# Kernel optimization log

Measured on AMD Instinct MI355X. Metric: run time of the kernel, lower is better.

## Reference

```python
import jax, jax.numpy as jnp
import numpy as np
import math

B, S, D, H = 2, 2048, 768, 12
DK = D // H


def setup_inputs() -> dict:
    key = jax.random.key(0)
    ks = jax.random.split(key, 8)
    scale = 1.0 / math.sqrt(D)  # xavier-ish scale for weights
    inp = {
        "query": jax.random.normal(ks[0], (B, S, D), jnp.float32),
        "key": jax.random.normal(ks[1], (B, S, D), jnp.float32),
        "value": jax.random.normal(ks[2], (B, S, D), jnp.float32),
        # causal mask: True = masked (matches torch masked_fill_ semantics)
        "mask": jnp.broadcast_to(jnp.triu(jnp.ones((S, S), bool), k=1), (B, S, S)),
        "wq": jax.random.normal(ks[3], (D, D), jnp.float32) * scale,
        "wk": jax.random.normal(ks[4], (D, D), jnp.float32) * scale,
        "wv": jax.random.normal(ks[5], (D, D), jnp.float32) * scale,
        "wo": jax.random.normal(ks[6], (D, D), jnp.float32) * scale,
        "bo": jnp.zeros((D,), jnp.float32),
    }
    return inp


def reference(query, key, value, mask, wq, wk, wv, wo, bo):
    # nn.Linear stores weight [out, in]; y = x @ W^T
    def split_heads(x):  # [B,S,D] -> [B,H,S,DK]
        return x.reshape(B, S, H, DK).transpose(0, 2, 1, 3)

    q = split_heads(jnp.einsum('bsd,ed->bse', query, wq))
    k = split_heads(jnp.einsum('bsd,ed->bse', key, wk))
    v = split_heads(jnp.einsum('bsd,ed->bse', value, wv))

    scores = jnp.einsum('bhqd,bhkd->bhqk', q, k) / math.sqrt(DK)
    scores = jnp.where(mask[:, None, :, :], -jnp.inf, scores)
    attn = jax.nn.softmax(scores, axis=-1)  # dropout is identity in eval / p=0

    attended = jnp.einsum('bhqk,bhkd->bhqd', attn, v)
    attended = attended.transpose(0, 2, 1, 3).reshape(B, S, D)
    return jnp.einsum('bsd,ed->bse', attended, wo) + bo
```

## Files before the change

### kernel.cpp

```cpp
#include <hip/hip_runtime.h>

namespace {
constexpr int Sc = 2048, Dc = 768, Hc = 12, Mc = 4096;

using fragb = __attribute__((ext_vector_type(8))) short;
using f32x4 = __attribute__((ext_vector_type(4))) float;

#define MFMA16(A, B, C) __builtin_amdgcn_mfma_f32_16x16x32_bf16(A, B, C, 0, 0, 0)

__device__ __forceinline__ unsigned short bf16rne(float f) {
  unsigned int u = __float_as_uint(f);
  return (unsigned short)((u + 0x7fffu + ((u >> 16) & 1u)) >> 16);
}
__device__ __forceinline__ void splitt(float f, unsigned short& h, unsigned short& l) {
  const unsigned int u = __float_as_uint(f);
  h = (unsigned short)(u >> 16);
  const float r = f - __uint_as_float(u & 0xffff0000u);
  l = (unsigned short)(__float_as_uint(r) >> 16);
}
__device__ __forceinline__ void gload16(const unsigned short* g, unsigned short* l) {
  __builtin_amdgcn_global_load_lds(
      (const __attribute__((address_space(1))) void*)g,
      (__attribute__((address_space(3))) void*)l, 16, 0, 0);
}

__global__ __launch_bounds__(256) void split_kernel(
    const float* __restrict__ src, unsigned short* __restrict__ h,
    unsigned short* __restrict__ l, int n8)
{
  const int i = blockIdx.x * 256 + threadIdx.x;
  if (i >= n8) return;
  const float4 v0 = *(const float4*)(src + (size_t)i * 8);
  const float4 v1 = *(const float4*)(src + (size_t)i * 8 + 4);
  const float x[8] = {v0.x, v0.y, v0.z, v0.w, v1.x, v1.y, v1.z, v1.w};
  unsigned short hh[8], ll[8];
#pragma unroll
  for (int j = 0; j < 8; ++j) splitt(x[j], hh[j], ll[j]);
  *(uint4*)&h[(size_t)i * 8] = *(const uint4*)&hh[0];
  *(uint4*)&l[(size_t)i * 8] = *(const uint4*)&ll[0];
}

template <int OMODE>
__global__ __launch_bounds__(256, 4) void proj_kernel(
    const unsigned short* __restrict__ Xh, const unsigned short* __restrict__ Xl,
    const float* __restrict__ W, const float* __restrict__ bias,
    unsigned short* __restrict__ Oh, unsigned short* __restrict__ Ol,
    float* __restrict__ Ofp)
{
  const int tid = threadIdx.x;
  const int lane = tid & 63, w = tid >> 6;
  const int g = lane >> 4, l15 = lane & 15;
  const int lrow = lane >> 2, lslot = lane & 3;
  const int m0 = blockIdx.x * 128, n0 = blockIdx.y * 64;

  __shared__ __align__(16) unsigned short sb[12288];

  f32x4 acc[2][4] = {};

  const int brow = tid >> 2;
  const int bcol = (tid & 3) * 8;
  const float* wp0 = W + (size_t)(n0 + brow) * Dc + bcol;

  for (int k0 = 0; k0 < Dc; k0 += 32) {
    unsigned int bpk[4], lpk[4];
    {
      const float* wp = wp0 + k0;
      const float4 v0 = *(const float4*)wp;
      const float4 v1 = *(const float4*)(wp + 4);
      const float x[8] = {v0.x, v0.y, v0.z, v0.w, v1.x, v1.y, v1.z, v1.w};
#pragma unroll
      for (int j = 0; j < 4; ++j) {
        unsigned short h0, l0, h1, l1;
        splitt(x[2*j], h0, l0); splitt(x[2*j+1], h1, l1);
        bpk[j] = (unsigned int)h0 | ((unsigned int)h1 << 16);
        lpk[j] = (unsigned int)l0 | ((unsigned int)l1 << 16);
      }
    }
    __syncthreads();
#pragma unroll
    for (int i = 0; i < 2; ++i) {
      const int q = 2 * w + i;
      const size_t goff = (size_t)(m0 + q * 16 + lrow) * Dc + k0 + lslot * 8;
      gload16(Xh + goff, &sb[q * 512]);
      gload16(Xl + goff, &sb[4096 + q * 512]);
    }
    *(uint4*)&sb[8192  + brow * 32 + bcol] = *(const uint4*)&bpk[0];
    *(uint4*)&sb[10240 + brow * 32 + bcol] = *(const uint4*)&lpk[0];
    __syncthreads();

    fragb bHf[4], bLf[4];
#pragma unroll
    for (int nb = 0; nb < 4; ++nb) {
      bHf[nb] = *(const fragb*)&sb[8192  + (nb * 16 + l15) * 32 + 8 * g];
      bLf[nb] = *(const fragb*)&sb[10240 + (nb * 16 + l15) * 32 + 8 * g];
    }
#pragma unroll
    for (int s = 0; s < 2; ++s) {
      const fragb aH = *(const fragb*)&sb[(32 * w + 16 * s + l15) * 32 + 8 * g];
      const fragb aL = *(const fragb*)&sb[4096 + (32 * w + 16 * s + l15) * 32 + 8 * g];
#pragma unroll
      for (int nb = 0; nb < 4; ++nb) {
        acc[s][nb] = MFMA16(aH, bHf[nb], acc[s][nb]);
        acc[s][nb] = MFMA16(aH, bLf[nb], acc[s][nb]);
        acc[s][nb] = MFMA16(aL, bHf[nb], acc[s][nb]);
      }
    }
  }

  if constexpr (OMODE == 2) {
#pragma unroll
    for (int s = 0; s < 2; ++s) {
      const int mrow = m0 + 32 * w + 16 * s + 4 * g;
#pragma unroll
      for (int nb = 0; nb < 4; ++nb) {
        const int n = n0 + nb * 16 + l15;
        const float bv = bias[n];
#pragma unroll
        for (int r = 0; r < 4; ++r)
          Ofp[(size_t)(mrow + r) * Dc + n] = acc[s][nb][r] + bv;
      }
    }
  } else {
    const int hsel = n0 >> 6;
    const int bb = m0 >> 11;
    const int sl0 = m0 & (Sc - 1);
#pragma unroll
    for (int pass = 0; pass < 2; ++pass) {
      __syncthreads();
#pragma unroll
      for (int s = 0; s < 2; ++s)
#pragma unroll
        for (int nb = 0; nb < 4; ++nb)
#pragma unroll
          for (int r = 0; r < 4; ++r) {
            unsigned short hv, lv;
            splitt(acc[s][nb][r], hv, lv);
            const int srow = 32 * w + 16 * s + 4 * g + r;
            const int dk = nb * 16 + l15;
            if (OMODE == 0) sb[srow * 64 + dk] = pass ? lv : hv;
            else            sb[dk * 128 + srow] = pass ? lv : hv;
          }
      __syncthreads();
      unsigned short* dst = pass ? Ol : Oh;
#pragma unroll
      for (int c2 = tid; c2 < 1024; c2 += 256) {
        size_t gidx;
        if (OMODE == 0) {
          const int sl = c2 >> 3, off = (c2 & 7) * 8;
          gidx = (((size_t)bb * Hc + hsel) * Sc + sl0 + sl) * 64 + off;
        } else {
          const int dk = c2 >> 4, off = (c2 & 15) * 8;
          gidx = (((size_t)bb * Hc + hsel) * 64 + dk) * Sc + sl0 + off;
        }
        *(uint4*)&dst[gidx] = *(const uint4*)&sb[c2 * 8];
      }
    }
  }
}

__global__ __launch_bounds__(256, 3) void attn_kernel(
    const unsigned short* __restrict__ Qh, const unsigned short* __restrict__ Ql,
    const unsigned short* __restrict__ Kh, const unsigned short* __restrict__ Kl,
    const unsigned short* __restrict__ Vth, const unsigned short* __restrict__ Vtl,
    unsigned short* __restrict__ Aoh, unsigned short* __restrict__ Aol)
{
  const int tid = threadIdx.x;
  const int lane = tid & 63, w = tid >> 6;
  const int g = lane >> 4, l15 = lane & 15;
  const int lrow = lane >> 2, lslot = lane & 3;
  const int t = blockIdx.x;
  const int bh = blockIdx.y;
  const int b = bh / Hc, h = bh % Hc;

  const int qtile = (w < 2) ? t : (63 - t);
  const int qbase = qtile * 32 + (w & 1) * 16;
  const int ktmax = (qbase + 15) >> 6;
  const int NKT = ((Sc - 1 - 32 * t) >> 6) + 1;

  __shared__ __align__(16) unsigned short sbuf[20992];

  const unsigned short* gbase;
  if      (w == 0) gbase = Kh  + (size_t)bh * Sc * 64;
  else if (w == 1) gbase = Kl  + (size_t)bh * Sc * 64;
  else if (w == 2) gbase = Vth + (size_t)bh * 64 * Sc;
  else             gbase = Vtl + (size_t)bh * 64 * Sc;
  const bool isK = (w < 2);

  fragb qfh[2], qfl[2];
  {
    const unsigned short* qrh = Qh + ((size_t)bh * Sc + qbase + l15) * 64;
    const unsigned short* qrl = Ql + ((size_t)bh * Sc + qbase + l15) * 64;
#pragma unroll
    for (int c = 0; c < 2; ++c) {
      qfh[c] = *(const fragb*)(qrh + c * 32 + g * 8);
      qfl[c] = *(const fragb*)(qrl + c * 32 + g * 8);
    }
  }

  f32x4 oacc[4] = {};
  float m_run[4] = {-1e30f, -1e30f, -1e30f, -1e30f};
  float l_run[4] = {0.f, 0.f, 0.f, 0.f};

  for (int kt = 0; kt < NKT; ++kt) {
    const int k0 = kt * 64;
    __syncthreads();
#pragma unroll
    for (int q = 0; q < 8; ++q) {
      const int cc = q >> 2, rb = (q & 3) * 16;
      const size_t off = isK
          ? ((size_t)(k0 + rb + lrow) * 64 + cc * 32 + lslot * 8)
          : ((size_t)(rb + lrow) * Sc + k0 + cc * 32 + lslot * 8);
      gload16(gbase + off, &sbuf[w * 4096 + q * 512]);
    }
    __syncthreads();

    if (kt <= ktmax) {
      f32x4 sacc[4] = {};
#pragma unroll
      for (int c = 0; c < 2; ++c) {
#pragma unroll
        for (int kb = 0; kb < 4; ++kb) {
          const fragb kH = *(const fragb*)&sbuf[c * 2048 + (kb * 16 + l15) * 32 + g * 8];
          const fragb kL = *(const fragb*)&sbuf[4096 + c * 2048 + (kb * 16 + l15) * 32 + g * 8];
          sacc[kb] = MFMA16(qfh[c], kH, sacc[kb]);
          sacc[kb] = MFMA16(qfh[c], kL, sacc[kb]);
          sacc[kb] = MFMA16(qfl[c], kH, sacc[kb]);
        }
      }
      float p[4][4], mx[4];
#pragma unroll
      for (int r = 0; r < 4; ++r) {
        const int qrow = qbase + 4 * g + r;
#pragma unroll
        for (int kb = 0; kb < 4; ++kb) {
          const int kc = k0 + kb * 16 + l15;
          const float x = sacc[kb][r] * 0.125f;
          p[kb][r] = (kc > qrow) ? -1e30f : x;
        }
        mx[r] = fmaxf(fmaxf(p[0][r], p[1][r]), fmaxf(p[2][r], p[3][r]));
      }
#pragma unroll
      for (int off = 8; off > 0; off >>= 1)
#pragma unroll
        for (int r = 0; r < 4; ++r)
          mx[r] = fmaxf(mx[r], __shfl_xor(mx[r], off));
#pragma unroll
      for (int r = 0; r < 4; ++r) {
        const float mnew = fmaxf(m_run[r], mx[r]);
        const float alpha = __expf(m_run[r] - mnew);
        m_run[r] = mnew;
        float rs = 0.f;
#pragma unroll
        for (int kb = 0; kb < 4; ++kb) { p[kb][r] = __expf(p[kb][r] - mnew); rs += p[kb][r]; }
#pragma unroll
        for (int off = 8; off > 0; off >>= 1) rs += __shfl_xor(rs, off);
        l_run[r] = l_run[r] * alpha + rs;
#pragma unroll
        for (int db = 0; db < 4; ++db) oacc[db][r] *= alpha;
      }
      const int strip = 16 * w;
#pragma unroll
      for (int kb = 0; kb < 4; ++kb)
#pragma unroll
        for (int r = 0; r < 4; ++r)
          sbuf[16384 + (strip + 4 * g + r) * 72 + kb * 16 + l15] = bf16rne(p[kb][r]);
#pragma unroll
      for (int c = 0; c < 2; ++c) {
        const fragb pf = *(const fragb*)&sbuf[16384 + (strip + l15) * 72 + c * 32 + g * 8];
#pragma unroll
        for (int db = 0; db < 4; ++db) {
          const fragb vH = *(const fragb*)&sbuf[8192  + c * 2048 + (db * 16 + l15) * 32 + g * 8];
          const fragb vL = *(const fragb*)&sbuf[12288 + c * 2048 + (db * 16 + l15) * 32 + g * 8];
          oacc[db] = MFMA16(pf, vH, oacc[db]);
          oacc[db] = MFMA16(pf, vL, oacc[db]);
        }
      }
    }
  }

#pragma unroll
  for (int r = 0; r < 4; ++r) {
    const float rl = 1.0f / l_run[r];
    const int s = qbase + 4 * g + r;
    const size_t base = ((size_t)b * Sc + s) * Dc + h * 64 + l15;
#pragma unroll
    for (int db = 0; db < 4; ++db) {
      unsigned short hbits, lbits;
      splitt(oacc[db][r] * rl, hbits, lbits);
      Aoh[base + db * 16] = hbits;
      Aol[base + db * 16] = lbits;
    }
  }
}

}

extern "C" void kernel_launch(void* const* d_in, const int* in_sizes, int n_in,
                              void* d_out, int out_size, void* d_ws, size_t ws_size,
                              hipStream_t stream) {
  const float* q  = (const float*)d_in[0];
  const float* k  = (const float*)d_in[1];
  const float* v  = (const float*)d_in[2];
  const float* wq = (const float*)d_in[4];
  const float* wk = (const float*)d_in[5];
  const float* wv = (const float*)d_in[6];
  const float* wo = (const float*)d_in[7];
  const float* bo = (const float*)d_in[8];

  unsigned short* ws = (unsigned short*)d_ws;
  const size_t NQ = (size_t)Mc * Dc;
  unsigned short* Xh_  = ws + 0 * NQ;
  unsigned short* Xl_  = ws + 1 * NQ;
  unsigned short* Qh_  = ws + 2 * NQ;
  unsigned short* Ql_  = ws + 3 * NQ;
  unsigned short* Kh_  = ws + 4 * NQ;
  unsigned short* Kl_  = ws + 5 * NQ;
  unsigned short* Vth_ = ws + 6 * NQ;
  unsigned short* Vtl_ = ws + 7 * NQ;

  const dim3 blk(256);
  const dim3 gsplit((Mc * Dc / 8 + 255) / 256);
  const dim3 gproj(Mc / 128, Dc / 64);
  const dim3 gattn(32, 2 * Hc);

  split_kernel<<<gsplit, blk, 0, stream>>>(q, Xh_, Xl_, Mc * Dc / 8);
  proj_kernel<0><<<gproj, blk, 0, stream>>>(Xh_, Xl_, wq, nullptr, Qh_, Ql_, nullptr);
  split_kernel<<<gsplit, blk, 0, stream>>>(k, Xh_, Xl_, Mc * Dc / 8);
  proj_kernel<0><<<gproj, blk, 0, stream>>>(Xh_, Xl_, wk, nullptr, Kh_, Kl_, nullptr);
  split_kernel<<<gsplit, blk, 0, stream>>>(v, Xh_, Xl_, Mc * Dc / 8);
  proj_kernel<1><<<gproj, blk, 0, stream>>>(Xh_, Xl_, wv, nullptr, Vth_, Vtl_, nullptr);
  attn_kernel<<<gattn, blk, 0, stream>>>(Qh_, Ql_, Kh_, Kl_, Vth_, Vtl_, Xh_, Xl_);
  proj_kernel<2><<<gproj, blk, 0, stream>>>(Xh_, Xl_, wo, bo, nullptr, nullptr, (float*)d_out);
}
```

Before: 349.5 us.

## Double-buffer LDS staging, XOR-swizzle shared layouts, and remap blocks for cache locality

Both the projection and attention kernels now use two LDS buffers, so the next K-tile's global-to-LDS loads are issued before computing on the current tile, and each iteration needs one barrier instead of two. Shared-memory tiles and the output staging buffers use an XOR swizzle to cut bank conflicts, and the 1D grids are remapped so neighbouring blocks spread across the XCDs with better L2 reuse. This doubles LDS use and lowers the occupancy hints (proj 4 to 3, attn 3 to 2). The projection output mode becomes a runtime argument instead of a template parameter.

```diff
diff --git a/kernel.cpp b/kernel.cpp
--- a/kernel.cpp
+++ b/kernel.cpp
@@ -18,7 +18,7 @@
   const float r = f - __uint_as_float(u & 0xffff0000u);
   l = (unsigned short)(__float_as_uint(r) >> 16);
 }
-__device__ __forceinline__ void gload16(const unsigned short* g, unsigned short* l) {
+__device__ __forceinline__ void gload16(const void* g, unsigned short* l) {
   __builtin_amdgcn_global_load_lds(
       (const __attribute__((address_space(1))) void*)g,
       (__attribute__((address_space(3))) void*)l, 16, 0, 0);
@@ -40,64 +40,61 @@
   *(uint4*)&l[(size_t)i * 8] = *(const uint4*)&ll[0];
 }
 
-template <int OMODE>
-__global__ __launch_bounds__(256, 4) void proj_kernel(
+__global__ __launch_bounds__(256, 3) void proj_kernel(
     const unsigned short* __restrict__ Xh, const unsigned short* __restrict__ Xl,
     const float* __restrict__ W, const float* __restrict__ bias,
     unsigned short* __restrict__ Oh, unsigned short* __restrict__ Ol,
-    float* __restrict__ Ofp)
+    float* __restrict__ Ofp, int omode)
 {
   const int tid = threadIdx.x;
   const int lane = tid & 63, w = tid >> 6;
   const int g = lane >> 4, l15 = lane & 15;
-  const int lrow = lane >> 2, lslot = lane & 3;
-  const int m0 = blockIdx.x * 128, n0 = blockIdx.y * 64;
-
-  __shared__ __align__(16) unsigned short sb[12288];
+  const int ar4 = lane >> 2, as4 = lane & 3;
+  const int asw = as4 ^ ((ar4 >> 1) & 3);
+  const int selr = (l15 >> 1) & 3;
+
+  const int bid = blockIdx.x;
+  const int swz = (bid & 7) * 48 + (bid >> 3);
+  const int m0 = (swz / 12) * 128, n0 = (swz % 12) * 64;
+
+  __shared__ __align__(16) unsigned short sb[24576];
 
   f32x4 acc[2][4] = {};
 
   const int brow = tid >> 2;
-  const int bcol = (tid & 3) * 8;
-  const float* wp0 = W + (size_t)(n0 + brow) * Dc + bcol;
-
-  for (int k0 = 0; k0 < Dc; k0 += 32) {
-    unsigned int bpk[4], lpk[4];
-    {
-      const float* wp = wp0 + k0;
-      const float4 v0 = *(const float4*)wp;
-      const float4 v1 = *(const float4*)(wp + 4);
-      const float x[8] = {v0.x, v0.y, v0.z, v0.w, v1.x, v1.y, v1.z, v1.w};
-#pragma unroll
-      for (int j = 0; j < 4; ++j) {
-        unsigned short h0, l0, h1, l1;
-        splitt(x[2*j], h0, l0); splitt(x[2*j+1], h1, l1);
-        bpk[j] = (unsigned int)h0 | ((unsigned int)h1 << 16);
-        lpk[j] = (unsigned int)l0 | ((unsigned int)l1 << 16);
-      }
-    }
-    __syncthreads();
+  const int bslot = (tid & 3) ^ ((tid >> 3) & 3);
+  const float* wp0 = W + (size_t)(n0 + brow) * Dc + (tid & 3) * 8;
+
+  auto stageA = [&](int k0, int bufb) {
 #pragma unroll
     for (int i = 0; i < 2; ++i) {
       const int q = 2 * w + i;
-      const size_t goff = (size_t)(m0 + q * 16 + lrow) * Dc + k0 + lslot * 8;
-      gload16(Xh + goff, &sb[q * 512]);
-      gload16(Xl + goff, &sb[4096 + q * 512]);
-    }
-    *(uint4*)&sb[8192  + brow * 32 + bcol] = *(const uint4*)&bpk[0];
-    *(uint4*)&sb[10240 + brow * 32 + bcol] = *(const uint4*)&lpk[0];
-    __syncthreads();
-
+      const size_t goff = (size_t)(m0 + q * 16 + ar4) * Dc + k0 + asw * 8;
+      gload16(Xh + goff, &sb[bufb + q * 512]);
+      gload16(Xl + goff, &sb[bufb + 4096 + q * 512]);
+    }
+  };
+  auto writeB = [&](const float4& f0, const float4& f1, int bufb) {
+    const float x[8] = {f0.x, f0.y, f0.z, f0.w, f1.x, f1.y, f1.z, f1.w};
+    unsigned short hh[8], ll[8];
+#pragma unroll
+    for (int j = 0; j < 8; ++j) splitt(x[j], hh[j], ll[j]);
+    *(uint4*)&sb[bufb + 8192  + brow * 32 + bslot * 8] = *(const uint4*)&hh[0];
+    *(uint4*)&sb[bufb + 10240 + brow * 32 + bslot * 8] = *(const uint4*)&ll[0];
+  };
+  auto compute = [&](int bufb) {
     fragb bHf[4], bLf[4];
 #pragma unroll
     for (int nb = 0; nb < 4; ++nb) {
-      bHf[nb] = *(const fragb*)&sb[8192  + (nb * 16 + l15) * 32 + 8 * g];
-      bLf[nb] = *(const fragb*)&sb[10240 + (nb * 16 + l15) * 32 + 8 * g];
+      const int ro = (nb * 16 + l15) * 32 + ((g ^ selr) * 8);
+      bHf[nb] = *(const fragb*)&sb[bufb + 8192 + ro];
+      bLf[nb] = *(const fragb*)&sb[bufb + 10240 + ro];
     }
 #pragma unroll
     for (int s = 0; s < 2; ++s) {
-      const fragb aH = *(const fragb*)&sb[(32 * w + 16 * s + l15) * 32 + 8 * g];
-      const fragb aL = *(const fragb*)&sb[4096 + (32 * w + 16 * s + l15) * 32 + 8 * g];
+      const int ro = (32 * w + 16 * s + l15) * 32 + ((g ^ selr) * 8);
+      const fragb aH = *(const fragb*)&sb[bufb + ro];
+      const fragb aL = *(const fragb*)&sb[bufb + 4096 + ro];
 #pragma unroll
       for (int nb = 0; nb < 4; ++nb) {
         acc[s][nb] = MFMA16(aH, bHf[nb], acc[s][nb]);
@@ -105,9 +102,32 @@
         acc[s][nb] = MFMA16(aL, bHf[nb], acc[s][nb]);
       }
     }
-  }
-
-  if constexpr (OMODE == 2) {
+  };
+
+  {
+    float4 f0 = *(const float4*)(wp0);
+    float4 f1 = *(const float4*)(wp0 + 4);
+    stageA(0, 0);
+    writeB(f0, f1, 0);
+  }
+  __syncthreads();
+  int cur = 0;
+  for (int t = 0; t < Dc / 32; ++t) {
+    const int nxt = cur ^ 1;
+    float4 f0, f1;
+    const bool more = (t + 1 < Dc / 32);
+    if (more) {
+      f0 = *(const float4*)(wp0 + (t + 1) * 32);
+      f1 = *(const float4*)(wp0 + (t + 1) * 32 + 4);
+      stageA((t + 1) * 32, nxt * 12288);
+    }
+    compute(cur * 12288);
+    if (more) writeB(f0, f1, nxt * 12288);
+    __syncthreads();
+    cur = nxt;
+  }
+
+  if (omode == 2) {
 #pragma unroll
     for (int s = 0; s < 2; ++s) {
       const int mrow = m0 + 32 * w + 16 * s + 4 * g;
@@ -121,9 +141,7 @@
       }
     }
   } else {
-    const int hsel = n0 >> 6;
-    const int bb = m0 >> 11;
-    const int sl0 = m0 & (Sc - 1);
+    const int hsel = n0 >> 6, bb = m0 >> 11, sl0 = m0 & (Sc - 1);
 #pragma unroll
     for (int pass = 0; pass < 2; ++pass) {
       __syncthreads();
@@ -137,28 +155,30 @@
             splitt(acc[s][nb][r], hv, lv);
             const int srow = 32 * w + 16 * s + 4 * g + r;
             const int dk = nb * 16 + l15;
-            if (OMODE == 0) sb[srow * 64 + dk] = pass ? lv : hv;
-            else            sb[dk * 128 + srow] = pass ? lv : hv;
+            if (omode == 0) sb[srow * 64 + (dk ^ ((srow & 7) << 3))] = pass ? lv : hv;
+            else            sb[dk * 128 + (srow ^ ((dk & 7) << 3))] = pass ? lv : hv;
           }
       __syncthreads();
       unsigned short* dst = pass ? Ol : Oh;
 #pragma unroll
       for (int c2 = tid; c2 < 1024; c2 += 256) {
-        size_t gidx;
-        if (OMODE == 0) {
-          const int sl = c2 >> 3, off = (c2 & 7) * 8;
-          gidx = (((size_t)bb * Hc + hsel) * Sc + sl0 + sl) * 64 + off;
+        size_t gidx; int src;
+        if (omode == 0) {
+          const int rr = c2 >> 3, pg = c2 & 7;
+          gidx = (((size_t)bb * Hc + hsel) * Sc + sl0 + rr) * 64 + ((pg ^ (rr & 7)) * 8);
+          src = c2 * 8;
         } else {
-          const int dk = c2 >> 4, off = (c2 & 15) * 8;
-          gidx = (((size_t)bb * Hc + hsel) * 64 + dk) * Sc + sl0 + off;
+          const int rr = c2 >> 4, pg = c2 & 15;
+          gidx = (((size_t)bb * Hc + hsel) * 64 + rr) * Sc + sl0 + ((pg ^ (rr & 7)) * 8);
+          src = c2 * 8;
         }
-        *(uint4*)&dst[gidx] = *(const uint4*)&sb[c2 * 8];
-      }
-    }
-  }
-}
-
-__global__ __launch_bounds__(256, 3) void attn_kernel(
+        *(uint4*)&dst[gidx] = *(const uint4*)&sb[src];
+      }
+    }
+  }
+}
+
+__global__ __launch_bounds__(256, 2) void attn_kernel(
     const unsigned short* __restrict__ Qh, const unsigned short* __restrict__ Ql,
     const unsigned short* __restrict__ Kh, const unsigned short* __restrict__ Kl,
     const unsigned short* __restrict__ Vth, const unsigned short* __restrict__ Vtl,
@@ -167,9 +187,13 @@
   const int tid = threadIdx.x;
   const int lane = tid & 63, w = tid >> 6;
   const int g = lane >> 4, l15 = lane & 15;
-  const int lrow = lane >> 2, lslot = lane & 3;
-  const int t = blockIdx.x;
-  const int bh = blockIdx.y;
+  const int ar4 = lane >> 2, as4 = lane & 3;
+  const int asw = as4 ^ ((ar4 >> 1) & 3);
+  const int selr = (l15 >> 1) & 3;
+
+  const int bid = blockIdx.x;
+  const int swz = (bid & 7) * 96 + (bid >> 3);
+  const int t = swz & 31, bh = swz >> 5;
   const int b = bh / Hc, h = bh % Hc;
 
   const int qtile = (w < 2) ? t : (63 - t);
@@ -177,7 +201,7 @@
   const int ktmax = (qbase + 15) >> 6;
   const int NKT = ((Sc - 1 - 32 * t) >> 6) + 1;
 
-  __shared__ __align__(16) unsigned short sbuf[20992];
+  __shared__ __align__(16) unsigned short sbuf[37376];
 
   const unsigned short* gbase;
   if      (w == 0) gbase = Kh  + (size_t)bh * Sc * 64;
@@ -186,6 +210,17 @@
   else             gbase = Vtl + (size_t)bh * 64 * Sc;
   const bool isK = (w < 2);
 
+  auto stage = [&](int k0, int bufb) {
+#pragma unroll
+    for (int q = 0; q < 8; ++q) {
+      const int cc = q >> 2, rb = (q & 3) * 16;
+      const size_t off = isK
+          ? ((size_t)(k0 + rb + ar4) * 64 + cc * 32 + asw * 8)
+          : ((size_t)(rb + ar4) * Sc + k0 + cc * 32 + asw * 8);
+      gload16(gbase + off, &sbuf[bufb + w * 4096 + q * 512]);
+    }
+  };
+
   fragb qfh[2], qfl[2];
   {
     const unsigned short* qrh = Qh + ((size_t)bh * Sc + qbase + l15) * 64;
@@ -201,27 +236,24 @@
   float m_run[4] = {-1e30f, -1e30f, -1e30f, -1e30f};
   float l_run[4] = {0.f, 0.f, 0.f, 0.f};
 
+  stage(0, 0);
+  __syncthreads();
+  int cur = 0;
   for (int kt = 0; kt < NKT; ++kt) {
     const int k0 = kt * 64;
-    __syncthreads();
-#pragma unroll
-    for (int q = 0; q < 8; ++q) {
-      const int cc = q >> 2, rb = (q & 3) * 16;
-      const size_t off = isK
-          ? ((size_t)(k0 + rb + lrow) * 64 + cc * 32 + lslot * 8)
-          : ((size_t)(rb + lrow) * Sc + k0 + cc * 32 + lslot * 8);
-      gload16(gbase + off, &sbuf[w * 4096 + q * 512]);
-    }
-    __syncthreads();
+    const int nxt = cur ^ 1;
+    if (kt + 1 < NKT) stage((kt + 1) * 64, nxt * 16384);
 
     if (kt <= ktmax) {
+      const int B = cur * 16384;
       f32x4 sacc[4] = {};
 #pragma unroll
       for (int c = 0; c < 2; ++c) {
 #pragma unroll
         for (int kb = 0; kb < 4; ++kb) {
-          const fragb kH = *(const fragb*)&sbuf[c * 2048 + (kb * 16 + l15) * 32 + g * 8];
-          const fragb kL = *(const fragb*)&sbuf[4096 + c * 2048 + (kb * 16 + l15) * 32 + g * 8];
+          const int ro = c * 2048 + (kb * 16 + l15) * 32 + ((g ^ selr) * 8);
+          const fragb kH = *(const fragb*)&sbuf[B + ro];
+          const fragb kL = *(const fragb*)&sbuf[B + 4096 + ro];
           sacc[kb] = MFMA16(qfh[c], kH, sacc[kb]);
           sacc[kb] = MFMA16(qfh[c], kL, sacc[kb]);
           sacc[kb] = MFMA16(qfl[c], kH, sacc[kb]);
@@ -263,19 +295,22 @@
       for (int kb = 0; kb < 4; ++kb)
 #pragma unroll
         for (int r = 0; r < 4; ++r)
-          sbuf[16384 + (strip + 4 * g + r) * 72 + kb * 16 + l15] = bf16rne(p[kb][r]);
+          sbuf[32768 + (strip + 4 * g + r) * 72 + kb * 16 + l15] = bf16rne(p[kb][r]);
 #pragma unroll
       for (int c = 0; c < 2; ++c) {
-        const fragb pf = *(const fragb*)&sbuf[16384 + (strip + l15) * 72 + c * 32 + g * 8];
+        const fragb pf = *(const fragb*)&sbuf[32768 + (strip + l15) * 72 + c * 32 + g * 8];
 #pragma unroll
         for (int db = 0; db < 4; ++db) {
-          const fragb vH = *(const fragb*)&sbuf[8192  + c * 2048 + (db * 16 + l15) * 32 + g * 8];
-          const fragb vL = *(const fragb*)&sbuf[12288 + c * 2048 + (db * 16 + l15) * 32 + g * 8];
+          const int ro = c * 2048 + (db * 16 + l15) * 32 + ((g ^ selr) * 8);
+          const fragb vH = *(const fragb*)&sbuf[B + 8192 + ro];
+          const fragb vL = *(const fragb*)&sbuf[B + 12288 + ro];
           oacc[db] = MFMA16(pf, vH, oacc[db]);
           oacc[db] = MFMA16(pf, vL, oacc[db]);
         }
       }
     }
+    __syncthreads();
+    cur = nxt;
   }
 
 #pragma unroll
@@ -319,16 +354,16 @@
   unsigned short* Vtl_ = ws + 7 * NQ;
 
   const dim3 blk(256);
-  const dim3 gsplit((Mc * Dc / 8 + 255) / 256);
-  const dim3 gproj(Mc / 128, Dc / 64);
-  const dim3 gattn(32, 2 * Hc);
+  const dim3 gsplit(Mc * Dc / 8 / 256);
+  const dim3 gproj(384);
+  const dim3 gattn(768);
 
   split_kernel<<<gsplit, blk, 0, stream>>>(q, Xh_, Xl_, Mc * Dc / 8);
-  proj_kernel<0><<<gproj, blk, 0, stream>>>(Xh_, Xl_, wq, nullptr, Qh_, Ql_, nullptr);
+  proj_kernel<<<gproj, blk, 0, stream>>>(Xh_, Xl_, wq, nullptr, Qh_, Ql_, nullptr, 0);
   split_kernel<<<gsplit, blk, 0, stream>>>(k, Xh_, Xl_, Mc * Dc / 8);
-  proj_kernel<0><<<gproj, blk, 0, stream>>>(Xh_, Xl_, wk, nullptr, Kh_, Kl_, nullptr);
+  proj_kernel<<<gproj, blk, 0, stream>>>(Xh_, Xl_, wk, nullptr, Kh_, Kl_, nullptr, 0);
   split_kernel<<<gsplit, blk, 0, stream>>>(v, Xh_, Xl_, Mc * Dc / 8);
-  proj_kernel<1><<<gproj, blk, 0, stream>>>(Xh_, Xl_, wv, nullptr, Vth_, Vtl_, nullptr);
+  proj_kernel<<<gproj, blk, 0, stream>>>(Xh_, Xl_, wv, nullptr, Vth_, Vtl_, nullptr, 1);
   attn_kernel<<<gattn, blk, 0, stream>>>(Qh_, Ql_, Kh_, Kl_, Vth_, Vtl_, Xh_, Xl_);
-  proj_kernel<2><<<gproj, blk, 0, stream>>>(Xh_, Xl_, wo, bo, nullptr, nullptr, (float*)d_out);
-}
+  proj_kernel<<<gproj, blk, 0, stream>>>(Xh_, Xl_, wo, bo, nullptr, nullptr, (float*)d_out, 2);
+}
```

Result: slower. 356.9 us (+2.1%).
